# Kernel tuning notes

Hardware: AMD Instinct MI355X
Metric: run time of the kernel (lower is better)

The kernel has to match this reference:

```python
import jax, jax.numpy as jnp
import numpy as np
from jax import lax

B, L, H, I, Z = 1024, 128, 256, 32, 128  # batch, max_length, hidden, input_size, latent


def setup_inputs() -> dict:
    key = jax.random.key(0)
    ks = jax.random.split(key, 32)
    p = lambda k, shape: (jax.random.normal(k, shape, dtype=jnp.float32) * 0.05)
    d = {
        "x": jax.random.normal(ks[0], (B, Z), dtype=jnp.float32),
        "W1": p(ks[1], (512, Z)), "b1": p(ks[2], (512,)),
        "W2": p(ks[3], (512, 512)), "b2": p(ks[4], (512,)),
        "W3": p(ks[5], (512, 512)), "b3": p(ks[6], (512,)),
        # predict_h / predict_c / predict_x_0 heads
        "Wh1": p(ks[7], (512, 512)), "bh1": p(ks[8], (512,)),
        "Wh2": p(ks[9], (H, 512)), "bh2": p(ks[10], (H,)),
        "Wc1": p(ks[11], (512, 512)), "bc1": p(ks[12], (512,)),
        "Wc2": p(ks[13], (H, 512)), "bc2": p(ks[14], (H,)),
        "Wx1": p(ks[15], (512, 512)), "bx1": p(ks[16], (512,)),
        "Wx2": p(ks[17], (H, 512)), "bx2": p(ks[18], (H,)),
        # decode LSTM (input H -> hidden H), PyTorch gate order i,f,g,o
        "rWih": p(ks[19], (4 * H, H)), "rWhh": p(ks[20], (4 * H, H)),
        "rbih": p(ks[21], (4 * H,)), "rbhh": p(ks[22], (4 * H,)),
        # predictor LSTM (input H -> hidden I)
        "pWih": p(ks[23], (4 * I, H)), "pWhh": p(ks[24], (4 * I, I)),
        "pbih": p(ks[25], (4 * I,)), "pbhh": p(ks[26], (4 * I,)),
    }
    return d


def _leaky(v):
    return jnp.where(v >= 0, v, 0.2 * v)


def _lstm_cell(xt, h, c, Wih, Whh, b):
    gates = xt @ Wih.T + h @ Whh.T + b  # [B, 4G]
    i, f, g, o = jnp.split(gates, 4, axis=-1)
    c_new = jax.nn.sigmoid(f) * c + jax.nn.sigmoid(i) * jnp.tanh(g)
    h_new = jax.nn.sigmoid(o) * jnp.tanh(c_new)
    return h_new, c_new


def _forward(x, W1, b1, W2, b2, W3, b3, Wh1, bh1, Wh2, bh2, Wc1, bc1, Wc2, bc2,
             Wx1, bx1, Wx2, bx2, rWih, rWhh, rbih, rbhh, pWih, pWhh, pbih, pbhh):
    t = _leaky(x @ W1.T + b1)
    t = _leaky(t @ W2.T + b2)
    t = _leaky(t @ W3.T + b3)
    h = _leaky(t @ Wh1.T + bh1) @ Wh2.T + bh2   # [B, H]
    c = _leaky(t @ Wc1.T + bc1) @ Wc2.T + bc2   # [B, H]
    x0 = _leaky(t @ Wx1.T + bx1) @ Wx2.T + bx2  # [B, H]

    rb = rbih + rbhh
    # The torch loop re-feeds the growing sequence through the LSTM from the
    # same initial (h, c) each step; deterministically this equals a single
    # O(L) self-feeding scan: token_{i} = h-output of step i, fed at step i+1.
    def dec_step(carry, _):
        tok, hh, cc = carry
        h2, c2 = _lstm_cell(tok, hh, cc, rWih, rWhh, rb)
        return (h2, h2, c2), h2

    _, outs = lax.scan(dec_step, (x0, h, c), None, length=L)  # [L, B, H]

    pb = pbih + pbhh
    def pred_step(carry, xt):
        hh, cc = carry
        hh, cc = _lstm_cell(xt, hh, cc, pWih, pWhh, pb)
        return (hh, cc), hh

    h0 = jnp.zeros((B, I), dtype=x.dtype)
    _, pouts = lax.scan(pred_step, (h0, h0), outs)  # [L, B, I]
    y = jnp.transpose(pouts, (1, 0, 2))  # [B, L, I]

    layer_type = jax.nn.softmax(y[..., : I - 1], axis=-1)
    features = jax.nn.sigmoid(y[..., I - 1:])
    return jnp.concatenate([layer_type, features], axis=-1)


def reference(x, W1, b1, W2, b2, W3, b3, Wh1, bh1, Wh2, bh2, Wc1, bc1, Wc2, bc2,
              Wx1, bx1, Wx2, bx2, rWih, rWhh, rbih, rbhh, pWih, pWhh, pbih, pbhh):
    return _forward(x, W1, b1, W2, b2, W3, b3, Wh1, bh1, Wh2, bh2, Wc1, bc1, Wc2, bc2,
                    Wx1, bx1, Wx2, bx2, rWih, rWhh, rbih, rbhh, pWih, pWhh, pbih, pbhh)
```

## Files before the change

kernel.cpp:

```cpp
#include <hip/hip_runtime.h>
#include <hip/hip_fp8.h>

typedef unsigned short u16;
typedef unsigned char u8;
typedef __attribute__((ext_vector_type(8))) __bf16 bfrag;
typedef long long f8frag;
typedef __attribute__((ext_vector_type(4))) float f32x4;

static __device__ __forceinline__ f32x4 MFMA(bfrag a, bfrag b, f32x4 c) {
  return __builtin_amdgcn_mfma_f32_16x16x32_bf16(a, b, c, 0, 0, 0);
}
static __device__ __forceinline__ f32x4 MFMA8(f8frag a, f8frag b, f32x4 c) {
  return __builtin_amdgcn_mfma_f32_16x16x32_fp8_fp8(a, b, c, 0, 0, 0);
}

static __device__ __forceinline__ u16 f2b(float f) {
  union { float f; unsigned u; } v; v.f = f;
  unsigned r = (v.u + 0x7fffu + ((v.u >> 16) & 1u)) >> 16;
  return (u16)r;
}
static __device__ __forceinline__ u8 f2e4m3(float f) {
  return (u8)(__builtin_amdgcn_cvt_pk_fp8_f32(f, f, 0, false) & 0xff);
}
static __device__ __forceinline__ unsigned pk4_e4m3(float a, float b, float c, float d) {
  int p = __builtin_amdgcn_cvt_pk_fp8_f32(a, b, 0, false);
  p = __builtin_amdgcn_cvt_pk_fp8_f32(c, d, p, true);
  return (unsigned)p;
}
static __device__ __forceinline__ float rcp(float x) { return __builtin_amdgcn_rcpf(x); }
static __device__ __forceinline__ float ssig(float x) {
  float E = __expf(x);
  return E * rcp(1.f + E);
}
static __device__ __forceinline__ float2 lstm2(float gi, float gf, float gg,
                                               float go, float c) {
  float Ei = __expf(gi), Ef = __expf(gf), Eg = __expf(2.f * gg), Eo = __expf(go);
  float P = 1.f + Ef, Q = 1.f + Ei, R = 1.f + Eg;
  float QR = Q * R;
  float num = c * Ef * QR + Ei * P * (Eg - 1.f);
  float cn = num * rcp(P * QR);
  float Ec = __expf(2.f * cn);
  float hn = Eo * (Ec - 1.f) * rcp((1.f + Eo) * (Ec + 1.f));
  return make_float2(hn, cn);
}

#define LDS_BARRIER() asm volatile("s_waitcnt lgkmcnt(0)\ns_barrier" ::: "memory")
#define PIN_A8(A) asm volatile("" : "+a"(A[0]), "+a"(A[1]), "+a"(A[2]), "+a"(A[3]), \
                                    "+a"(A[4]), "+a"(A[5]), "+a"(A[6]), "+a"(A[7]))
#define PIN_V8(A) asm volatile("" : "+v"(A[0]), "+v"(A[1]), "+v"(A[2]), "+v"(A[3]), \
                                    "+v"(A[4]), "+v"(A[5]), "+v"(A[6]), "+v"(A[7]))

struct PrepArgs {
  const float *x, *W1, *W2, *W3, *Wh1, *Wc1, *Wx1, *Wh2, *Wc2, *Wx2;
  const float *rWih, *rWhh, *rbih, *rbhh, *pWih, *pWhh, *pbih, *pbhh;
  u16 *Xbf, *W1b, *W2b, *W3b, *Wh1b, *Wc1b, *Wx1b, *Wh2b, *Wc2b, *Wx2b;
  u16 *WcatR;
  u8 *WsS, *pWsS, *pWhhS;
  float *rbR, *pbR;
};

static __device__ __forceinline__ void emit_stream(u16* dst, const float* src,
                                                   int i, int K, int ktbits) {
  int j = i & 7, lane = (i >> 3) & 63;
  int kt = (i >> 9) & ((1 << ktbits) - 1);
  int nt = (i >> (9 + ktbits)) & 3;
  int ct = i >> (11 + ktbits);
  int srow = ct * 64 + nt * 16 + (lane & 15);
  int scol = kt * 32 + ((lane >> 4) & 3) * 8 + j;
  dst[i] = f2b(src[srow * K + scol]);
}

__global__ __launch_bounds__(256) void prep(PrepArgs p) {
  const int tid0 = blockIdx.x * 256 + threadIdx.x;
  const int stride = gridDim.x * 256;
  switch (blockIdx.y) {
    case 0: for (int i = tid0; i < 131072; i += stride) p.Xbf[i] = f2b(p.x[i]); break;
    case 1: for (int i = tid0; i < 65536;  i += stride) emit_stream(p.W1b, p.W1, i, 128, 2); break;
    case 2: for (int i = tid0; i < 262144; i += stride) emit_stream(p.W2b, p.W2, i, 512, 4); break;
    case 3: for (int i = tid0; i < 262144; i += stride) emit_stream(p.W3b, p.W3, i, 512, 4); break;
    case 4: for (int i = tid0; i < 262144; i += stride) emit_stream(p.Wh1b, p.Wh1, i, 512, 4); break;
    case 5: for (int i = tid0; i < 262144; i += stride) emit_stream(p.Wc1b, p.Wc1, i, 512, 4); break;
    case 6: for (int i = tid0; i < 262144; i += stride) emit_stream(p.Wx1b, p.Wx1, i, 512, 4); break;
    case 7: for (int i = tid0; i < 131072; i += stride) emit_stream(p.Wh2b, p.Wh2, i, 512, 4); break;
    case 8: for (int i = tid0; i < 131072; i += stride) emit_stream(p.Wc2b, p.Wc2, i, 512, 4); break;
    case 9: for (int i = tid0; i < 131072; i += stride) emit_stream(p.Wx2b, p.Wx2, i, 512, 4); break;
    case 10:
      for (int i = tid0; i < 524288; i += stride) {
        int j = i & 7, lane = (i >> 3) & 63, kt = (i >> 9) & 15;
        int gate = (i >> 13) & 3, w16 = i >> 15;
        int srow = gate * 256 + w16 * 16 + (lane & 15);
        int k = kt * 32 + ((lane >> 4) & 3) * 8 + j;
        float v = (k < 256) ? p.rWih[srow * 256 + k] : p.rWhh[srow * 256 + (k - 256)];
        p.WcatR[i] = f2b(v);
      }
      break;
    case 11:
      for (int i = tid0; i < 1024; i += stride) {
        int srow = (((i >> 4) & 3) << 8) + ((i >> 6) << 4) + (i & 15);
        p.rbR[i] = p.rbih[srow] + p.rbhh[srow];
      }
      break;
    case 12:
      for (int i = tid0; i < 32768; i += stride) {
        int j = i & 7, lane = (i >> 3) & 63, kt = (i >> 9) & 7, w = i >> 12;
        int n = w * 16 + (lane & 15);
        int srow = ((n & 3) << 5) + (n >> 2);
        int k = kt * 32 + ((lane >> 4) & 3) * 8 + j;
        p.pWsS[i] = f2e4m3(p.pWih[srow * 256 + k]);
      }
      break;
    case 13:
      for (int i = tid0; i < 4096; i += stride) {
        int j = i & 7, lane = (i >> 3) & 63, w = i >> 9;
        int n = w * 16 + (lane & 15);
        int srow = ((n & 3) << 5) + (n >> 2);
        int k = ((lane >> 4) & 3) * 8 + j;
        p.pWhhS[i] = f2e4m3(p.pWhh[srow * 32 + k]);
      }
      break;
    case 14:
      for (int i = tid0; i < 128; i += stride) {
        int srow = ((i & 3) << 5) + (i >> 2);
        p.pbR[i] = p.pbih[srow] + p.pbhh[srow];
      }
      break;
    case 15:
      for (int i = tid0; i < 262144; i += stride) {
        int j = i & 7, lane = (i >> 3) & 63, kt = (i >> 9) & 7;
        int gate = (i >> 12) & 3, g16 = i >> 14;
        int srow = gate * 256 + g16 * 16 + (lane & 15);
        int k = kt * 32 + ((lane >> 4) & 3) * 8 + j;
        p.WsS[i] = f2e4m3(p.rWih[srow * 256 + k] + p.rWhh[srow * 256 + k]);
      }
      break;
  }
}

__global__ __launch_bounds__(256) void gemm_act(
    const u16* __restrict__ X, const u16* __restrict__ W,
    const float* __restrict__ bias,
    u16* __restrict__ Yb, float* __restrict__ Yf,
    int K, int ldo, int coloff, int leaky) {
  const int rt = blockIdx.x, ct = blockIdx.y;
  const int lane = threadIdx.x & 63, wave = threadIdx.x >> 6;
  const int m15 = lane & 15, q = lane >> 4, kq = q * 8;
  const int KT = K >> 5;
  const int row = rt * 64 + wave * 16 + m15;
  f32x4 acc[4] = {};
  const u16* xp = X + (size_t)row * K + kq;
  const u16* wst = W + lane * 8;
  for (int kt = 0; kt < KT; kt++) {
    bfrag a = *(const bfrag*)(xp + kt * 32);
#pragma unroll
    for (int nt = 0; nt < 4; nt++) {
      const u16* wp = wst + (size_t)((ct * 4 + nt) * KT + kt) * 512;
      acc[nt] = MFMA(a, *(const bfrag*)wp, acc[nt]);
    }
  }
#pragma unroll
  for (int nt = 0; nt < 4; nt++) {
    int col = ct * 64 + nt * 16 + m15;
    float bv = bias[col];
#pragma unroll
    for (int r = 0; r < 4; r++) {
      int orow = rt * 64 + wave * 16 + q * 4 + r;
      float v = acc[nt][r] + bv;
      if (leaky) v = v >= 0.f ? v : 0.2f * v;
      if (Yb) Yb[(size_t)orow * ldo + coloff + col] = f2b(v);
      else    Yf[(size_t)orow * ldo + coloff + col] = v;
    }
  }
}

struct G3 {
  const u16 *X, *W;
  const float* bias;
  u16* Yb;
  float* Yf;
  int K, ldo, coloff, leaky;
};
__global__ __launch_bounds__(256) void gemm_act3(G3 ga, G3 gb, G3 gc) {
  G3 g = (blockIdx.z == 0) ? ga : (blockIdx.z == 1) ? gb : gc;
  const int rt = blockIdx.x, ct = blockIdx.y;
  const int lane = threadIdx.x & 63, wave = threadIdx.x >> 6;
  const int m15 = lane & 15, q = lane >> 4, kq = q * 8;
  const int KT = g.K >> 5;
  const int row = rt * 64 + wave * 16 + m15;
  f32x4 acc[4] = {};
  const u16* xp = g.X + (size_t)row * g.K + kq;
  const u16* wst = g.W + lane * 8;
  for (int kt = 0; kt < KT; kt++) {
    bfrag a = *(const bfrag*)(xp + kt * 32);
#pragma unroll
    for (int nt = 0; nt < 4; nt++) {
      const u16* wp = wst + (size_t)((ct * 4 + nt) * KT + kt) * 512;
      acc[nt] = MFMA(a, *(const bfrag*)wp, acc[nt]);
    }
  }
#pragma unroll
  for (int nt = 0; nt < 4; nt++) {
    int col = ct * 64 + nt * 16 + m15;
    float bv = g.bias[col];
#pragma unroll
    for (int r = 0; r < 4; r++) {
      int orow = rt * 64 + wave * 16 + q * 4 + r;
      float v = acc[nt][r] + bv;
      if (g.leaky) v = v >= 0.f ? v : 0.2f * v;
      if (g.Yb) g.Yb[(size_t)orow * g.ldo + g.coloff + col] = f2b(v);
      else      g.Yf[(size_t)orow * g.ldo + g.coloff + col] = v;
    }
  }
}

__global__ __attribute__((amdgpu_flat_work_group_size(1024, 1024), amdgpu_waves_per_eu(4, 4)))
void decode_h(
    const u8* __restrict__ WsS,
    const u16* __restrict__ WcatR,
    const float* __restrict__ rb,
    const float* __restrict__ CB,
    const u16* __restrict__ X0H,
    u8* __restrict__ hG) {
  __shared__ __align__(16) u8 hbufS[2][4096];
  __shared__ __align__(16) u8 WoL[16][4096];
  const int tid = threadIdx.x;
  const int w = tid >> 6, lane = tid & 63;
  const int m15 = lane & 15, q = lane >> 4;
  const int b = blockIdx.x;
  const int rowg = b * 16;

  {
    int4* dst = (int4*)WoL;
    for (int i = tid; i < 4096; i += 1024) {
      int wv = i >> 8, rest = i & 255;
      dst[i] = ((const int4*)(WsS + wv * 16384 + 12288))[rest];
    }
  }
  const float* rbp = rb + w * 64 + q * 4;
  f32x4 rbv0 = *(const f32x4*)(rbp +  0);
  f32x4 rbv1 = *(const f32x4*)(rbp + 16);
  f32x4 rbv2 = *(const f32x4*)(rbp + 32);
  f32x4 rbv3 = *(const f32x4*)(rbp + 48);
  asm volatile("" : "+v"(rbv0), "+v"(rbv1), "+v"(rbv2), "+v"(rbv3));
  f32x4 cst = *(const f32x4*)(CB + (size_t)(rowg + m15) * 256 + w * 16 + q * 4);
  const int wroff = (w >> 1) * 512 + ((w & 1) * 2 + (q >> 1)) * 128 + m15 * 8 + (q & 1) * 4;
  u8* hGs = hG + (size_t)b * 524288 + wroff;

  {
    f32x4 ai = rbv0, af_ = rbv1, ag = rbv2, ao = rbv3;
    const u16* xrow = X0H + (size_t)(rowg + m15) * 512 + q * 8;
    const u16* wcw = WcatR + (size_t)w * 32768 + lane * 8;
#pragma unroll
    for (int kt = 0; kt < 16; kt++) {
      bfrag a = *(const bfrag*)(xrow + kt * 32);
      ai  = MFMA(*(const bfrag*)(wcw + kt * 512), a, ai);
      af_ = MFMA(*(const bfrag*)(wcw + 8192 + kt * 512), a, af_);
      ag  = MFMA(*(const bfrag*)(wcw + 16384 + kt * 512), a, ag);
      ao  = MFMA(*(const bfrag*)(wcw + 24576 + kt * 512), a, ao);
    }
    float hn[4];
#pragma unroll
    for (int r = 0; r < 4; r++) {
      float2 hc2 = lstm2(ai[r], af_[r], ag[r], ao[r], cst[r]);
      hn[r] = hc2.x;
      cst[r] = hc2.y;
    }
    unsigned hv = pk4_e4m3(hn[0], hn[1], hn[2], hn[3]);
    *(unsigned*)(&hbufS[0][wroff]) = hv;
    *(unsigned*)hGs = hv;
  }
  const u8* wsb = WsS + (size_t)w * 16384 + lane * 8;
  f8frag Wv0[8], Wv1[8], Wv2[8];
#pragma unroll
  for (int kt = 0; kt < 8; kt++) {
    Wv0[kt] = *(const f8frag*)(wsb + kt * 512);
    Wv1[kt] = *(const f8frag*)(wsb + 4096 + kt * 512);
    Wv2[kt] = *(const f8frag*)(wsb + 8192 + kt * 512);
  }
  PIN_A8(Wv0); PIN_A8(Wv1); PIN_A8(Wv2);
  const u8* woW = &WoL[w][lane * 8];
  __syncthreads();

  for (int s = 1; s < 128; s++) {
    PIN_A8(Wv0); PIN_A8(Wv1); PIN_A8(Wv2);
    asm volatile("" : "+v"(rbv0), "+v"(rbv1), "+v"(rbv2), "+v"(rbv3));
    const u8* h8 = &hbufS[(s - 1) & 1][lane * 8];
    f32x4 ai = rbv0, af_ = rbv1, ag = rbv2, ao = rbv3;
#pragma unroll
    for (int kt = 0; kt < 8; kt++) {
      f8frag a8 = *(const f8frag*)(h8 + kt * 512);
      f8frag wo = *(const f8frag*)(woW + kt * 512);
      ai  = MFMA8(Wv0[kt], a8, ai);
      af_ = MFMA8(Wv1[kt], a8, af_);
      ag  = MFMA8(Wv2[kt], a8, ag);
      ao  = MFMA8(wo, a8, ao);
    }
    float hn[4];
#pragma unroll
    for (int r = 0; r < 4; r++) {
      float2 hc2 = lstm2(ai[r], af_[r], ag[r], ao[r], cst[r]);
      hn[r] = hc2.x;
      cst[r] = hc2.y;
    }
    unsigned hv = pk4_e4m3(hn[0], hn[1], hn[2], hn[3]);
    *(unsigned*)(&hbufS[s & 1][wroff]) = hv;
    *(unsigned*)(hGs + (size_t)s * 4096) = hv;
    LDS_BARRIER();
  }
}

__global__ __launch_bounds__(512, 2) void pred_y(
    const u8* __restrict__ hG,
    const u8* __restrict__ pWsS,
    const u8* __restrict__ pWhhS,
    const float* __restrict__ pb,
    float* __restrict__ out) {
  __shared__ __align__(16) u8 stageL[16384];
  __shared__ __align__(16) u8 hp8[2][16][40];
  __shared__ float ysC[4][16][36];
  const int tid = threadIdx.x;
  const int w = tid >> 6, lane = tid & 63;
  const int m15 = lane & 15, q = lane >> 4;
  const int b = blockIdx.x, rowg = b * 16;
  for (int i = tid; i < 2 * 16 * 40; i += 512) (&hp8[0][0][0])[i] = 0;
  const u8* pwsb = pWsS + (size_t)w * 4096 + lane * 8;
  f8frag pbv[8];
#pragma unroll
  for (int kt = 0; kt < 8; kt++) pbv[kt] = *(const f8frag*)(pwsb + kt * 512);
  f8frag phw = *(const f8frag*)(pWhhS + (size_t)w * 512 + lane * 8);
  PIN_V8(pbv);
  asm volatile("" : "+v"(phw));
  const f32x4 pbias = *(const f32x4*)(pb + w * 16 + q * 4);
  float cp = 0.f;
  const int4* hGb = (const int4*)(hG + (size_t)b * 524288);
  const int t_si = (tid >> 3) >> 4, t_r = (tid >> 3) & 15, sub = tid & 7;
  __syncthreads();

  for (int cs = 0; cs < 32; cs++) {
    {
      int4* sdst = (int4*)stageL;
      sdst[tid] = hGb[cs * 1024 + tid];
      sdst[tid + 512] = hGb[cs * 1024 + tid + 512];
    }
    __syncthreads();
#pragma unroll
    for (int si = 0; si < 4; si++) {
      const int s = cs * 4 + si;
      const u8* xr8 = &stageL[si * 4096 + lane * 8];
      f32x4 pacc = pbias;
#pragma unroll
      for (int kt = 0; kt < 8; kt++) {
        f8frag pav = *(const f8frag*)(xr8 + kt * 512);
        pacc = MFMA8(pbv[kt], pav, pacc);
      }
      f8frag pah = *(const f8frag*)(&hp8[s & 1][m15][q * 8]);
      pacc = MFMA8(phw, pah, pacc);
      float2 hc2 = lstm2(pacc[0], pacc[1], pacc[2], pacc[3], cp);
      cp = hc2.y;
      hp8[(s + 1) & 1][m15][w * 4 + q] = f2e4m3(hc2.x);
      ysC[si][m15][w * 4 + q] = hc2.x;
      LDS_BARRIER();
    }
    {
      f32x4 yv = *(const f32x4*)&ysC[t_si][t_r][sub * 4];
      float v3 = (sub == 7) ? -1e30f : yv[3];
      float m = fmaxf(fmaxf(yv[0], yv[1]), fmaxf(yv[2], v3));
#pragma unroll
      for (int off = 4; off; off >>= 1) m = fmaxf(m, __shfl_xor(m, off, 8));
      float e0 = __expf(yv[0] - m), e1 = __expf(yv[1] - m), e2 = __expf(yv[2] - m);
      float e3 = (sub == 7) ? 0.f : __expf(yv[3] - m);
      float tot = e0 + e1 + e2 + e3;
#pragma unroll
      for (int off = 4; off; off >>= 1) tot += __shfl_xor(tot, off, 8);
      float inv = rcp(tot);
      f32x4 o;
      o[0] = e0 * inv; o[1] = e1 * inv; o[2] = e2 * inv;
      o[3] = (sub == 7) ? ssig(yv[3]) : e3 * inv;
      *(f32x4*)(out + (size_t)(rowg + t_r) * 4096 + (cs * 4 + t_si) * 32 + sub * 4) = o;
    }
    LDS_BARRIER();
  }
}

extern "C" void kernel_launch(void* const* d_in, const int* in_sizes, int n_in,
                              void* d_out, int out_size, void* d_ws, size_t ws_size,
                              hipStream_t stream) {
  (void)in_sizes; (void)n_in; (void)out_size; (void)ws_size;
  const float* x    = (const float*)d_in[0];
  const float* W1   = (const float*)d_in[1];
  const float* b1   = (const float*)d_in[2];
  const float* W2   = (const float*)d_in[3];
  const float* b2   = (const float*)d_in[4];
  const float* W3   = (const float*)d_in[5];
  const float* b3   = (const float*)d_in[6];
  const float* Wh1  = (const float*)d_in[7];
  const float* bh1  = (const float*)d_in[8];
  const float* Wh2  = (const float*)d_in[9];
  const float* bh2  = (const float*)d_in[10];
  const float* Wc1  = (const float*)d_in[11];
  const float* bc1  = (const float*)d_in[12];
  const float* Wc2  = (const float*)d_in[13];
  const float* bc2  = (const float*)d_in[14];
  const float* Wx1  = (const float*)d_in[15];
  const float* bx1  = (const float*)d_in[16];
  const float* Wx2  = (const float*)d_in[17];
  const float* bx2  = (const float*)d_in[18];
  const float* rWih = (const float*)d_in[19];
  const float* rWhh = (const float*)d_in[20];
  const float* rbih = (const float*)d_in[21];
  const float* rbhh = (const float*)d_in[22];
  const float* pWih = (const float*)d_in[23];
  const float* pWhh = (const float*)d_in[24];
  const float* pbih = (const float*)d_in[25];
  const float* pbhh = (const float*)d_in[26];

  char* w = (char*)d_ws;
  auto alloc = [&](size_t bytes) -> char* {
    char* p = w;
    w += (bytes + 255) & ~(size_t)255;
    return p;
  };
  u16* Xbf  = (u16*)alloc(1024 * 128 * 2);
  u16* T1   = (u16*)alloc(1024 * 512 * 2);
  u16* T2   = (u16*)alloc(1024 * 512 * 2);
  u16* T3   = (u16*)alloc(1024 * 512 * 2);
  u16* TH   = (u16*)alloc(1024 * 512 * 2);
  u16* TC   = (u16*)alloc(1024 * 512 * 2);
  u16* TX   = (u16*)alloc(1024 * 512 * 2);
  u16* X0H  = (u16*)alloc(1024 * 512 * 2);
  float* CB = (float*)alloc(1024 * 256 * 4);
  u16* W1b  = (u16*)alloc(512 * 128 * 2);
  u16* W2b  = (u16*)alloc(512 * 512 * 2);
  u16* W3b  = (u16*)alloc(512 * 512 * 2);
  u16* Wh1b = (u16*)alloc(512 * 512 * 2);
  u16* Wc1b = (u16*)alloc(512 * 512 * 2);
  u16* Wx1b = (u16*)alloc(512 * 512 * 2);
  u16* Wh2b = (u16*)alloc(256 * 512 * 2);
  u16* Wc2b = (u16*)alloc(256 * 512 * 2);
  u16* Wx2b = (u16*)alloc(256 * 512 * 2);
  u16* WcatR= (u16*)alloc(1024 * 512 * 2);
  u8*  WsS  = (u8*)alloc(262144);
  u8*  pWsS = (u8*)alloc(32768);
  u8*  pWhhS= (u8*)alloc(4096);
  float* rbR = (float*)alloc(1024 * 4);
  float* pbR = (float*)alloc(128 * 4);
  u8*  hG   = (u8*)alloc((size_t)64 * 128 * 4096);

  PrepArgs pa;
  pa.x = x; pa.W1 = W1; pa.W2 = W2; pa.W3 = W3; pa.Wh1 = Wh1; pa.Wc1 = Wc1; pa.Wx1 = Wx1;
  pa.Wh2 = Wh2; pa.Wc2 = Wc2; pa.Wx2 = Wx2;
  pa.rWih = rWih; pa.rWhh = rWhh; pa.rbih = rbih; pa.rbhh = rbhh;
  pa.pWih = pWih; pa.pWhh = pWhh; pa.pbih = pbih; pa.pbhh = pbhh;
  pa.Xbf = Xbf; pa.W1b = W1b; pa.W2b = W2b; pa.W3b = W3b; pa.Wh1b = Wh1b;
  pa.Wc1b = Wc1b; pa.Wx1b = Wx1b; pa.Wh2b = Wh2b; pa.Wc2b = Wc2b; pa.Wx2b = Wx2b;
  pa.WcatR = WcatR;
  pa.WsS = WsS; pa.pWsS = pWsS; pa.pWhhS = pWhhS;
  pa.rbR = rbR; pa.pbR = pbR;
  prep<<<dim3(32, 16), 256, 0, stream>>>(pa);

  gemm_act<<<dim3(16, 8), 256, 0, stream>>>(Xbf, W1b, b1, T1, nullptr, 128, 512, 0, 1);
  gemm_act<<<dim3(16, 8), 256, 0, stream>>>(T1, W2b, b2, T2, nullptr, 512, 512, 0, 1);
  gemm_act<<<dim3(16, 8), 256, 0, stream>>>(T2, W3b, b3, T3, nullptr, 512, 512, 0, 1);
  G3 h1a = {T3, Wh1b, bh1, TH, nullptr, 512, 512, 0, 1};
  G3 h1b = {T3, Wc1b, bc1, TC, nullptr, 512, 512, 0, 1};
  G3 h1c = {T3, Wx1b, bx1, TX, nullptr, 512, 512, 0, 1};
  gemm_act3<<<dim3(16, 8, 3), 256, 0, stream>>>(h1a, h1b, h1c);
  G3 h2a = {TH, Wh2b, bh2, X0H, nullptr, 512, 512, 256, 0};
  G3 h2b = {TC, Wc2b, bc2, nullptr, CB, 512, 256, 0, 0};
  G3 h2c = {TX, Wx2b, bx2, X0H, nullptr, 512, 512, 0, 0};
  gemm_act3<<<dim3(16, 4, 3), 256, 0, stream>>>(h2a, h2b, h2c);

  decode_h<<<64, 1024, 0, stream>>>(WsS, WcatR, rbR, CB, X0H, hG);
  pred_y<<<64, 512, 0, stream>>>(hG, pWsS, pWhhS, pbR, (float*)d_out);
}
```

Before: 487.3 us.

## Fuse MLP trunk and heads into decode kernel using swizzled LDS activations

Removes the five separate GEMM launches and instead computes the whole MLP trunk plus the h/c/x0 heads inside the decode_h kernel. Each block handles its 16 rows, and intermediate activations ping-pong through XOR-swizzled shared-memory buffers instead of global memory. The initial c state stays in registers, and the x0/h concatenation is written straight to LDS. This saves launch overhead and global round trips. In exchange, only 64 blocks do all the MLP work, so every block re-reads all the MLP weights from global or cache.

```diff
diff --git a/kernel.cpp b/kernel.cpp
--- a/kernel.cpp
+++ b/kernel.cpp
@@ -6,6 +6,7 @@
 typedef __attribute__((ext_vector_type(8))) __bf16 bfrag;
 typedef long long f8frag;
 typedef __attribute__((ext_vector_type(4))) float f32x4;
+typedef __attribute__((ext_vector_type(4))) unsigned short u16x4;
 
 static __device__ __forceinline__ f32x4 MFMA(bfrag a, bfrag b, f32x4 c) {
   return __builtin_amdgcn_mfma_f32_16x16x32_bf16(a, b, c, 0, 0, 0);
@@ -49,6 +50,10 @@
                                     "+a"(A[4]), "+a"(A[5]), "+a"(A[6]), "+a"(A[7]))
 #define PIN_V8(A) asm volatile("" : "+v"(A[0]), "+v"(A[1]), "+v"(A[2]), "+v"(A[3]), \
                                     "+v"(A[4]), "+v"(A[5]), "+v"(A[6]), "+v"(A[7]))
+
+static __device__ __forceinline__ int sw(int r, int byteoff) {
+  return r * 1024 + (byteoff ^ ((r & 7) << 4));
+}
 
 struct PrepArgs {
   const float *x, *W1, *W2, *W3, *Wh1, *Wc1, *Wx1, *Wh2, *Wc2, *Wx2;
@@ -136,92 +141,64 @@
   }
 }
 
-__global__ __launch_bounds__(256) void gemm_act(
-    const u16* __restrict__ X, const u16* __restrict__ W,
+template<int NT, int KT, bool AG, bool OL>
+static __device__ __forceinline__ void mlayer(
+    const u16* __restrict__ Ag,
+    const u8* __restrict__ Al,
+    u8* __restrict__ Ol,
+    int cobyte,
+    f32x4* accOut,
+    const u16* __restrict__ Wst,
     const float* __restrict__ bias,
-    u16* __restrict__ Yb, float* __restrict__ Yf,
-    int K, int ldo, int coloff, int leaky) {
-  const int rt = blockIdx.x, ct = blockIdx.y;
-  const int lane = threadIdx.x & 63, wave = threadIdx.x >> 6;
-  const int m15 = lane & 15, q = lane >> 4, kq = q * 8;
-  const int KT = K >> 5;
-  const int row = rt * 64 + wave * 16 + m15;
-  f32x4 acc[4] = {};
-  const u16* xp = X + (size_t)row * K + kq;
-  const u16* wst = W + lane * 8;
+    int w, int m15, int q, int leaky) {
+  f32x4 acc[NT];
+#pragma unroll
+  for (int nt = 0; nt < NT; nt++)
+    acc[nt] = *(const f32x4*)(bias + (w * NT + nt) * 16 + q * 4);
+#pragma unroll
   for (int kt = 0; kt < KT; kt++) {
-    bfrag a = *(const bfrag*)(xp + kt * 32);
-#pragma unroll
-    for (int nt = 0; nt < 4; nt++) {
-      const u16* wp = wst + (size_t)((ct * 4 + nt) * KT + kt) * 512;
-      acc[nt] = MFMA(a, *(const bfrag*)wp, acc[nt]);
-    }
-  }
-#pragma unroll
-  for (int nt = 0; nt < 4; nt++) {
-    int col = ct * 64 + nt * 16 + m15;
-    float bv = bias[col];
-#pragma unroll
-    for (int r = 0; r < 4; r++) {
-      int orow = rt * 64 + wave * 16 + q * 4 + r;
-      float v = acc[nt][r] + bv;
-      if (leaky) v = v >= 0.f ? v : 0.2f * v;
-      if (Yb) Yb[(size_t)orow * ldo + coloff + col] = f2b(v);
-      else    Yf[(size_t)orow * ldo + coloff + col] = v;
-    }
-  }
-}
-
-struct G3 {
-  const u16 *X, *W;
-  const float* bias;
-  u16* Yb;
-  float* Yf;
-  int K, ldo, coloff, leaky;
+    bfrag a;
+    if (AG) a = *(const bfrag*)(Ag + kt * 32);
+    else    a = *(const bfrag*)(Al + sw(m15, kt * 64 + q * 16));
+#pragma unroll
+    for (int nt = 0; nt < NT; nt++) {
+      bfrag wv = *(const bfrag*)(Wst + (size_t)(((w * NT + nt) * KT + kt) << 9));
+      acc[nt] = MFMA(wv, a, acc[nt]);
+    }
+  }
+#pragma unroll
+  for (int nt = 0; nt < NT; nt++) {
+    if (leaky) {
+#pragma unroll
+      for (int r = 0; r < 4; r++)
+        acc[nt][r] = acc[nt][r] >= 0.f ? acc[nt][r] : 0.2f * acc[nt][r];
+    }
+    if (OL) {
+      u16x4 pk;
+#pragma unroll
+      for (int r = 0; r < 4; r++) pk[r] = f2b(acc[nt][r]);
+      *(u16x4*)(Ol + sw(m15, cobyte + ((w * NT + nt) * 16 + q * 4) * 2)) = pk;
+    } else {
+      accOut[nt] = acc[nt];
+    }
+  }
+}
+
+struct MegaArgs {
+  const u8* WsS; const u16* WcatR; const float* rb;
+  const u16* Xbf;
+  const u16 *W1b, *W2b, *W3b, *Wh1b, *Wh2b, *Wc1b, *Wc2b, *Wx1b, *Wx2b;
+  const float *b1, *b2, *b3, *bh1, *bh2, *bc1, *bc2, *bx1, *bx2;
+  u8* hG;
 };
-__global__ __launch_bounds__(256) void gemm_act3(G3 ga, G3 gb, G3 gc) {
-  G3 g = (blockIdx.z == 0) ? ga : (blockIdx.z == 1) ? gb : gc;
-  const int rt = blockIdx.x, ct = blockIdx.y;
-  const int lane = threadIdx.x & 63, wave = threadIdx.x >> 6;
-  const int m15 = lane & 15, q = lane >> 4, kq = q * 8;
-  const int KT = g.K >> 5;
-  const int row = rt * 64 + wave * 16 + m15;
-  f32x4 acc[4] = {};
-  const u16* xp = g.X + (size_t)row * g.K + kq;
-  const u16* wst = g.W + lane * 8;
-  for (int kt = 0; kt < KT; kt++) {
-    bfrag a = *(const bfrag*)(xp + kt * 32);
-#pragma unroll
-    for (int nt = 0; nt < 4; nt++) {
-      const u16* wp = wst + (size_t)((ct * 4 + nt) * KT + kt) * 512;
-      acc[nt] = MFMA(a, *(const bfrag*)wp, acc[nt]);
-    }
-  }
-#pragma unroll
-  for (int nt = 0; nt < 4; nt++) {
-    int col = ct * 64 + nt * 16 + m15;
-    float bv = g.bias[col];
-#pragma unroll
-    for (int r = 0; r < 4; r++) {
-      int orow = rt * 64 + wave * 16 + q * 4 + r;
-      float v = acc[nt][r] + bv;
-      if (g.leaky) v = v >= 0.f ? v : 0.2f * v;
-      if (g.Yb) g.Yb[(size_t)orow * g.ldo + g.coloff + col] = f2b(v);
-      else      g.Yf[(size_t)orow * g.ldo + g.coloff + col] = v;
-    }
-  }
-}
 
 __global__ __attribute__((amdgpu_flat_work_group_size(1024, 1024), amdgpu_waves_per_eu(4, 4)))
-void decode_h(
-    const u8* __restrict__ WsS,
-    const u16* __restrict__ WcatR,
-    const float* __restrict__ rb,
-    const float* __restrict__ CB,
-    const u16* __restrict__ X0H,
-    u8* __restrict__ hG) {
+void decode_h(MegaArgs p) {
   __shared__ __align__(16) u8 hbufS[2][4096];
   __shared__ __align__(16) u8 WoL[16][4096];
+  __shared__ __align__(16) u8 bufA[16384];
+  __shared__ __align__(16) u8 bufB[16384];
+  __shared__ __align__(16) u8 xh[16384];
   const int tid = threadIdx.x;
   const int w = tid >> 6, lane = tid & 63;
   const int m15 = lane & 15, q = lane >> 4;
@@ -232,26 +209,61 @@
     int4* dst = (int4*)WoL;
     for (int i = tid; i < 4096; i += 1024) {
       int wv = i >> 8, rest = i & 255;
-      dst[i] = ((const int4*)(WsS + wv * 16384 + 12288))[rest];
-    }
-  }
-  const float* rbp = rb + w * 64 + q * 4;
+      dst[i] = ((const int4*)(p.WsS + wv * 16384 + 12288))[rest];
+    }
+  }
+
+  const u16* wl8 = (const u16*)nullptr;
+  f32x4 cst;
+  {
+    const u16* Ag1 = p.Xbf + (size_t)(rowg + m15) * 128 + q * 8;
+    mlayer<2, 4, true, true>(Ag1, nullptr, bufA, 0, nullptr,
+                             p.W1b + lane * 8, p.b1, w, m15, q, 1);
+    LDS_BARRIER();
+    mlayer<2, 16, false, true>(nullptr, bufA, bufB, 0, nullptr,
+                               p.W2b + lane * 8, p.b2, w, m15, q, 1);
+    LDS_BARRIER();
+    mlayer<2, 16, false, true>(nullptr, bufB, bufA, 0, nullptr,
+                               p.W3b + lane * 8, p.b3, w, m15, q, 1);
+    LDS_BARRIER();
+    mlayer<2, 16, false, true>(nullptr, bufA, bufB, 0, nullptr,
+                               p.Wh1b + lane * 8, p.bh1, w, m15, q, 1);
+    LDS_BARRIER();
+    mlayer<1, 16, false, true>(nullptr, bufB, xh, 512, nullptr,
+                               p.Wh2b + lane * 8, p.bh2, w, m15, q, 0);
+    LDS_BARRIER();
+    mlayer<2, 16, false, true>(nullptr, bufA, bufB, 0, nullptr,
+                               p.Wc1b + lane * 8, p.bc1, w, m15, q, 1);
+    LDS_BARRIER();
+    f32x4 cacc[1];
+    mlayer<1, 16, false, false>(nullptr, bufB, nullptr, 0, cacc,
+                                p.Wc2b + lane * 8, p.bc2, w, m15, q, 0);
+    cst = cacc[0];
+    LDS_BARRIER();
+    mlayer<2, 16, false, true>(nullptr, bufA, bufB, 0, nullptr,
+                               p.Wx1b + lane * 8, p.bx1, w, m15, q, 1);
+    LDS_BARRIER();
+    mlayer<1, 16, false, true>(nullptr, bufB, xh, 0, nullptr,
+                               p.Wx2b + lane * 8, p.bx2, w, m15, q, 0);
+    LDS_BARRIER();
+  }
+  (void)wl8;
+
+  const float* rbp = p.rb + w * 64 + q * 4;
   f32x4 rbv0 = *(const f32x4*)(rbp +  0);
   f32x4 rbv1 = *(const f32x4*)(rbp + 16);
   f32x4 rbv2 = *(const f32x4*)(rbp + 32);
   f32x4 rbv3 = *(const f32x4*)(rbp + 48);
   asm volatile("" : "+v"(rbv0), "+v"(rbv1), "+v"(rbv2), "+v"(rbv3));
-  f32x4 cst = *(const f32x4*)(CB + (size_t)(rowg + m15) * 256 + w * 16 + q * 4);
   const int wroff = (w >> 1) * 512 + ((w & 1) * 2 + (q >> 1)) * 128 + m15 * 8 + (q & 1) * 4;
-  u8* hGs = hG + (size_t)b * 524288 + wroff;
+  u8* hGs = p.hG + (size_t)b * 524288 + wroff;
 
   {
     f32x4 ai = rbv0, af_ = rbv1, ag = rbv2, ao = rbv3;
-    const u16* xrow = X0H + (size_t)(rowg + m15) * 512 + q * 8;
-    const u16* wcw = WcatR + (size_t)w * 32768 + lane * 8;
+    const u16* wcw = p.WcatR + (size_t)w * 32768 + lane * 8;
 #pragma unroll
     for (int kt = 0; kt < 16; kt++) {
-      bfrag a = *(const bfrag*)(xrow + kt * 32);
+      bfrag a = *(const bfrag*)(xh + sw(m15, kt * 64 + q * 16));
       ai  = MFMA(*(const bfrag*)(wcw + kt * 512), a, ai);
       af_ = MFMA(*(const bfrag*)(wcw + 8192 + kt * 512), a, af_);
       ag  = MFMA(*(const bfrag*)(wcw + 16384 + kt * 512), a, ag);
@@ -268,7 +280,7 @@
     *(unsigned*)(&hbufS[0][wroff]) = hv;
     *(unsigned*)hGs = hv;
   }
-  const u8* wsb = WsS + (size_t)w * 16384 + lane * 8;
+  const u8* wsb = p.WsS + (size_t)w * 16384 + lane * 8;
   f8frag Wv0[8], Wv1[8], Wv2[8];
 #pragma unroll
   for (int kt = 0; kt < 8; kt++) {
@@ -420,14 +432,6 @@
     return p;
   };
   u16* Xbf  = (u16*)alloc(1024 * 128 * 2);
-  u16* T1   = (u16*)alloc(1024 * 512 * 2);
-  u16* T2   = (u16*)alloc(1024 * 512 * 2);
-  u16* T3   = (u16*)alloc(1024 * 512 * 2);
-  u16* TH   = (u16*)alloc(1024 * 512 * 2);
-  u16* TC   = (u16*)alloc(1024 * 512 * 2);
-  u16* TX   = (u16*)alloc(1024 * 512 * 2);
-  u16* X0H  = (u16*)alloc(1024 * 512 * 2);
-  float* CB = (float*)alloc(1024 * 256 * 4);
   u16* W1b  = (u16*)alloc(512 * 128 * 2);
   u16* W2b  = (u16*)alloc(512 * 512 * 2);
   u16* W3b  = (u16*)alloc(512 * 512 * 2);
@@ -457,18 +461,16 @@
   pa.rbR = rbR; pa.pbR = pbR;
   prep<<<dim3(32, 16), 256, 0, stream>>>(pa);
 
-  gemm_act<<<dim3(16, 8), 256, 0, stream>>>(Xbf, W1b, b1, T1, nullptr, 128, 512, 0, 1);
-  gemm_act<<<dim3(16, 8), 256, 0, stream>>>(T1, W2b, b2, T2, nullptr, 512, 512, 0, 1);
-  gemm_act<<<dim3(16, 8), 256, 0, stream>>>(T2, W3b, b3, T3, nullptr, 512, 512, 0, 1);
-  G3 h1a = {T3, Wh1b, bh1, TH, nullptr, 512, 512, 0, 1};
-  G3 h1b = {T3, Wc1b, bc1, TC, nullptr, 512, 512, 0, 1};
-  G3 h1c = {T3, Wx1b, bx1, TX, nullptr, 512, 512, 0, 1};
-  gemm_act3<<<dim3(16, 8, 3), 256, 0, stream>>>(h1a, h1b, h1c);
-  G3 h2a = {TH, Wh2b, bh2, X0H, nullptr, 512, 512, 256, 0};
-  G3 h2b = {TC, Wc2b, bc2, nullptr, CB, 512, 256, 0, 0};
-  G3 h2c = {TX, Wx2b, bx2, X0H, nullptr, 512, 512, 0, 0};
-  gemm_act3<<<dim3(16, 4, 3), 256, 0, stream>>>(h2a, h2b, h2c);
-
-  decode_h<<<64, 1024, 0, stream>>>(WsS, WcatR, rbR, CB, X0H, hG);
+  MegaArgs ma;
+  ma.WsS = WsS; ma.WcatR = WcatR; ma.rb = rbR;
+  ma.Xbf = Xbf;
+  ma.W1b = W1b; ma.W2b = W2b; ma.W3b = W3b;
+  ma.Wh1b = Wh1b; ma.Wh2b = Wh2b; ma.Wc1b = Wc1b; ma.Wc2b = Wc2b;
+  ma.Wx1b = Wx1b; ma.Wx2b = Wx2b;
+  ma.b1 = b1; ma.b2 = b2; ma.b3 = b3; ma.bh1 = bh1; ma.bh2 = bh2;
+  ma.bc1 = bc1; ma.bc2 = bc2; ma.bx1 = bx1; ma.bx2 = bx2;
+  ma.hG = hG;
+
+  decode_h<<<64, 1024, 0, stream>>>(ma);
   pred_y<<<64, 512, 0, stream>>>(hG, pWsS, pWhhS, pbR, (float*)d_out);
 }
```

Measured after the change: 532.3 us. 9.2% more time.

## Fuse decode and predictor LSTMs into one kernel with flag-based producer/consumer overlap

Applied to the files above, without the earlier changes.

Merges the decode LSTM and predictor LSTM kernels into a single 128-block launch. Blocks 0-63 run the decode recurrence and publish a per-block progress flag every four steps. Blocks 64-127 spin on that flag and consume the hidden states while decoding is still running, so the two sequential recurrences overlap instead of running back to back. This depends on all 128 blocks being co-resident, or the spin-waits deadlock. It also adds atomic loads and stores, and the predictor blocks now run at 1024 threads with half the waves idle.

```diff
diff --git a/kernel.cpp b/kernel.cpp
--- a/kernel.cpp
+++ b/kernel.cpp
@@ -57,6 +57,7 @@
   u16 *WcatR;
   u8 *WsS, *pWsS, *pWhhS;
   float *rbR, *pbR;
+  unsigned *flags;
 };
 
 static __device__ __forceinline__ void emit_stream(u16* dst, const float* src,
@@ -123,6 +124,8 @@
         int srow = ((i & 3) << 5) + (i >> 2);
         p.pbR[i] = p.pbih[srow] + p.pbhh[srow];
       }
+      for (int i = tid0; i < 64; i += stride)
+        __hip_atomic_store(p.flags + i, 0u, __ATOMIC_RELAXED, __HIP_MEMORY_SCOPE_AGENT);
       break;
     case 15:
       for (int i = tid0; i < 262144; i += stride) {
@@ -213,171 +216,188 @@
 }
 
 __global__ __attribute__((amdgpu_flat_work_group_size(1024, 1024), amdgpu_waves_per_eu(4, 4)))
-void decode_h(
+void decode_pred(
     const u8* __restrict__ WsS,
     const u16* __restrict__ WcatR,
     const float* __restrict__ rb,
     const float* __restrict__ CB,
     const u16* __restrict__ X0H,
-    u8* __restrict__ hG) {
-  __shared__ __align__(16) u8 hbufS[2][4096];
-  __shared__ __align__(16) u8 WoL[16][4096];
-  const int tid = threadIdx.x;
-  const int w = tid >> 6, lane = tid & 63;
-  const int m15 = lane & 15, q = lane >> 4;
-  const int b = blockIdx.x;
-  const int rowg = b * 16;
-
-  {
-    int4* dst = (int4*)WoL;
-    for (int i = tid; i < 4096; i += 1024) {
-      int wv = i >> 8, rest = i & 255;
-      dst[i] = ((const int4*)(WsS + wv * 16384 + 12288))[rest];
-    }
-  }
-  const float* rbp = rb + w * 64 + q * 4;
-  f32x4 rbv0 = *(const f32x4*)(rbp +  0);
-  f32x4 rbv1 = *(const f32x4*)(rbp + 16);
-  f32x4 rbv2 = *(const f32x4*)(rbp + 32);
-  f32x4 rbv3 = *(const f32x4*)(rbp + 48);
-  asm volatile("" : "+v"(rbv0), "+v"(rbv1), "+v"(rbv2), "+v"(rbv3));
-  f32x4 cst = *(const f32x4*)(CB + (size_t)(rowg + m15) * 256 + w * 16 + q * 4);
-  const int wroff = (w >> 1) * 512 + ((w & 1) * 2 + (q >> 1)) * 128 + m15 * 8 + (q & 1) * 4;
-  u8* hGs = hG + (size_t)b * 524288 + wroff;
-
-  {
-    f32x4 ai = rbv0, af_ = rbv1, ag = rbv2, ao = rbv3;
-    const u16* xrow = X0H + (size_t)(rowg + m15) * 512 + q * 8;
-    const u16* wcw = WcatR + (size_t)w * 32768 + lane * 8;
-#pragma unroll
-    for (int kt = 0; kt < 16; kt++) {
-      bfrag a = *(const bfrag*)(xrow + kt * 32);
-      ai  = MFMA(*(const bfrag*)(wcw + kt * 512), a, ai);
-      af_ = MFMA(*(const bfrag*)(wcw + 8192 + kt * 512), a, af_);
-      ag  = MFMA(*(const bfrag*)(wcw + 16384 + kt * 512), a, ag);
-      ao  = MFMA(*(const bfrag*)(wcw + 24576 + kt * 512), a, ao);
-    }
-    float hn[4];
-#pragma unroll
-    for (int r = 0; r < 4; r++) {
-      float2 hc2 = lstm2(ai[r], af_[r], ag[r], ao[r], cst[r]);
-      hn[r] = hc2.x;
-      cst[r] = hc2.y;
-    }
-    unsigned hv = pk4_e4m3(hn[0], hn[1], hn[2], hn[3]);
-    *(unsigned*)(&hbufS[0][wroff]) = hv;
-    *(unsigned*)hGs = hv;
-  }
-  const u8* wsb = WsS + (size_t)w * 16384 + lane * 8;
-  f8frag Wv0[8], Wv1[8], Wv2[8];
-#pragma unroll
-  for (int kt = 0; kt < 8; kt++) {
-    Wv0[kt] = *(const f8frag*)(wsb + kt * 512);
-    Wv1[kt] = *(const f8frag*)(wsb + 4096 + kt * 512);
-    Wv2[kt] = *(const f8frag*)(wsb + 8192 + kt * 512);
-  }
-  PIN_A8(Wv0); PIN_A8(Wv1); PIN_A8(Wv2);
-  const u8* woW = &WoL[w][lane * 8];
-  __syncthreads();
-
-  for (int s = 1; s < 128; s++) {
-    PIN_A8(Wv0); PIN_A8(Wv1); PIN_A8(Wv2);
-    asm volatile("" : "+v"(rbv0), "+v"(rbv1), "+v"(rbv2), "+v"(rbv3));
-    const u8* h8 = &hbufS[(s - 1) & 1][lane * 8];
-    f32x4 ai = rbv0, af_ = rbv1, ag = rbv2, ao = rbv3;
-#pragma unroll
-    for (int kt = 0; kt < 8; kt++) {
-      f8frag a8 = *(const f8frag*)(h8 + kt * 512);
-      f8frag wo = *(const f8frag*)(woW + kt * 512);
-      ai  = MFMA8(Wv0[kt], a8, ai);
-      af_ = MFMA8(Wv1[kt], a8, af_);
-      ag  = MFMA8(Wv2[kt], a8, ag);
-      ao  = MFMA8(wo, a8, ao);
-    }
-    float hn[4];
-#pragma unroll
-    for (int r = 0; r < 4; r++) {
-      float2 hc2 = lstm2(ai[r], af_[r], ag[r], ao[r], cst[r]);
-      hn[r] = hc2.x;
-      cst[r] = hc2.y;
-    }
-    unsigned hv = pk4_e4m3(hn[0], hn[1], hn[2], hn[3]);
-    *(unsigned*)(&hbufS[s & 1][wroff]) = hv;
-    *(unsigned*)(hGs + (size_t)s * 4096) = hv;
-    LDS_BARRIER();
-  }
-}
-
-__global__ __launch_bounds__(512, 2) void pred_y(
-    const u8* __restrict__ hG,
     const u8* __restrict__ pWsS,
     const u8* __restrict__ pWhhS,
     const float* __restrict__ pb,
-    float* __restrict__ out) {
+    float* __restrict__ out,
+    u8* __restrict__ hG,
+    unsigned* __restrict__ flags) {
+  __shared__ __align__(16) u8 hbufS[2][4096];
+  __shared__ __align__(16) u8 WoL[16][4096];
   __shared__ __align__(16) u8 stageL[16384];
   __shared__ __align__(16) u8 hp8[2][16][40];
   __shared__ float ysC[4][16][36];
   const int tid = threadIdx.x;
   const int w = tid >> 6, lane = tid & 63;
   const int m15 = lane & 15, q = lane >> 4;
-  const int b = blockIdx.x, rowg = b * 16;
-  for (int i = tid; i < 2 * 16 * 40; i += 512) (&hp8[0][0][0])[i] = 0;
-  const u8* pwsb = pWsS + (size_t)w * 4096 + lane * 8;
-  f8frag pbv[8];
-#pragma unroll
-  for (int kt = 0; kt < 8; kt++) pbv[kt] = *(const f8frag*)(pwsb + kt * 512);
-  f8frag phw = *(const f8frag*)(pWhhS + (size_t)w * 512 + lane * 8);
-  PIN_V8(pbv);
-  asm volatile("" : "+v"(phw));
-  const f32x4 pbias = *(const f32x4*)(pb + w * 16 + q * 4);
-  float cp = 0.f;
-  const int4* hGb = (const int4*)(hG + (size_t)b * 524288);
-  const int t_si = (tid >> 3) >> 4, t_r = (tid >> 3) & 15, sub = tid & 7;
-  __syncthreads();
-
-  for (int cs = 0; cs < 32; cs++) {
+
+  if (blockIdx.x < 64) {
+    const int b = blockIdx.x;
+    const int rowg = b * 16;
     {
-      int4* sdst = (int4*)stageL;
-      sdst[tid] = hGb[cs * 1024 + tid];
-      sdst[tid + 512] = hGb[cs * 1024 + tid + 512];
-    }
+      int4* dst = (int4*)WoL;
+      for (int i = tid; i < 4096; i += 1024) {
+        int wv = i >> 8, rest = i & 255;
+        dst[i] = ((const int4*)(WsS + wv * 16384 + 12288))[rest];
+      }
+    }
+    const float* rbp = rb + w * 64 + q * 4;
+    f32x4 rbv0 = *(const f32x4*)(rbp +  0);
+    f32x4 rbv1 = *(const f32x4*)(rbp + 16);
+    f32x4 rbv2 = *(const f32x4*)(rbp + 32);
+    f32x4 rbv3 = *(const f32x4*)(rbp + 48);
+    asm volatile("" : "+v"(rbv0), "+v"(rbv1), "+v"(rbv2), "+v"(rbv3));
+    f32x4 cst = *(const f32x4*)(CB + (size_t)(rowg + m15) * 256 + w * 16 + q * 4);
+    const int wroff = (w >> 1) * 512 + ((w & 1) * 2 + (q >> 1)) * 128 + m15 * 8 + (q & 1) * 4;
+    u8* hGs = hG + (size_t)b * 524288 + wroff;
+
+    {
+      f32x4 ai = rbv0, af_ = rbv1, ag = rbv2, ao = rbv3;
+      const u16* xrow = X0H + (size_t)(rowg + m15) * 512 + q * 8;
+      const u16* wcw = WcatR + (size_t)w * 32768 + lane * 8;
+#pragma unroll
+      for (int kt = 0; kt < 16; kt++) {
+        bfrag a = *(const bfrag*)(xrow + kt * 32);
+        ai  = MFMA(*(const bfrag*)(wcw + kt * 512), a, ai);
+        af_ = MFMA(*(const bfrag*)(wcw + 8192 + kt * 512), a, af_);
+        ag  = MFMA(*(const bfrag*)(wcw + 16384 + kt * 512), a, ag);
+        ao  = MFMA(*(const bfrag*)(wcw + 24576 + kt * 512), a, ao);
+      }
+      float hn[4];
+#pragma unroll
+      for (int r = 0; r < 4; r++) {
+        float2 hc2 = lstm2(ai[r], af_[r], ag[r], ao[r], cst[r]);
+        hn[r] = hc2.x;
+        cst[r] = hc2.y;
+      }
+      unsigned hv = pk4_e4m3(hn[0], hn[1], hn[2], hn[3]);
+      *(unsigned*)(&hbufS[0][wroff]) = hv;
+      __hip_atomic_store((unsigned*)hGs, hv, __ATOMIC_RELAXED, __HIP_MEMORY_SCOPE_AGENT);
+    }
+    const u8* wsb = WsS + (size_t)w * 16384 + lane * 8;
+    f8frag Wv0[8], Wv1[8], Wv2[8];
+#pragma unroll
+    for (int kt = 0; kt < 8; kt++) {
+      Wv0[kt] = *(const f8frag*)(wsb + kt * 512);
+      Wv1[kt] = *(const f8frag*)(wsb + 4096 + kt * 512);
+      Wv2[kt] = *(const f8frag*)(wsb + 8192 + kt * 512);
+    }
+    PIN_A8(Wv0); PIN_A8(Wv1); PIN_A8(Wv2);
+    const u8* woW = &WoL[w][lane * 8];
     __syncthreads();
-#pragma unroll
-    for (int si = 0; si < 4; si++) {
-      const int s = cs * 4 + si;
-      const u8* xr8 = &stageL[si * 4096 + lane * 8];
-      f32x4 pacc = pbias;
+
+    for (int s = 1; s < 128; s++) {
+      PIN_A8(Wv0); PIN_A8(Wv1); PIN_A8(Wv2);
+      asm volatile("" : "+v"(rbv0), "+v"(rbv1), "+v"(rbv2), "+v"(rbv3));
+      const u8* h8 = &hbufS[(s - 1) & 1][lane * 8];
+      f32x4 ai = rbv0, af_ = rbv1, ag = rbv2, ao = rbv3;
 #pragma unroll
       for (int kt = 0; kt < 8; kt++) {
-        f8frag pav = *(const f8frag*)(xr8 + kt * 512);
-        pacc = MFMA8(pbv[kt], pav, pacc);
-      }
-      f8frag pah = *(const f8frag*)(&hp8[s & 1][m15][q * 8]);
-      pacc = MFMA8(phw, pah, pacc);
-      float2 hc2 = lstm2(pacc[0], pacc[1], pacc[2], pacc[3], cp);
-      cp = hc2.y;
-      hp8[(s + 1) & 1][m15][w * 4 + q] = f2e4m3(hc2.x);
-      ysC[si][m15][w * 4 + q] = hc2.x;
+        f8frag a8 = *(const f8frag*)(h8 + kt * 512);
+        f8frag wo = *(const f8frag*)(woW + kt * 512);
+        ai  = MFMA8(Wv0[kt], a8, ai);
+        af_ = MFMA8(Wv1[kt], a8, af_);
+        ag  = MFMA8(Wv2[kt], a8, ag);
+        ao  = MFMA8(wo, a8, ao);
+      }
+      float hn[4];
+#pragma unroll
+      for (int r = 0; r < 4; r++) {
+        float2 hc2 = lstm2(ai[r], af_[r], ag[r], ao[r], cst[r]);
+        hn[r] = hc2.x;
+        cst[r] = hc2.y;
+      }
+      unsigned hv = pk4_e4m3(hn[0], hn[1], hn[2], hn[3]);
+      *(unsigned*)(&hbufS[s & 1][wroff]) = hv;
+      __hip_atomic_store((unsigned*)(hGs + (size_t)s * 4096), hv,
+                         __ATOMIC_RELAXED, __HIP_MEMORY_SCOPE_AGENT);
+      if ((s & 3) == 3) {
+        __syncthreads();
+        if (tid == 0)
+          __hip_atomic_store(flags + b, (unsigned)((s >> 2) + 1),
+                             __ATOMIC_RELEASE, __HIP_MEMORY_SCOPE_AGENT);
+      } else {
+        LDS_BARRIER();
+      }
+    }
+  } else {
+    const int b = blockIdx.x - 64;
+    const int rowg = b * 16;
+    for (int i = tid; i < 2 * 16 * 40; i += 1024) (&hp8[0][0][0])[i] = 0;
+    const u8* pwsb = pWsS + (size_t)(w & 7) * 4096 + lane * 8;
+    f8frag pbv[8];
+#pragma unroll
+    for (int kt = 0; kt < 8; kt++) pbv[kt] = *(const f8frag*)(pwsb + kt * 512);
+    f8frag phw = *(const f8frag*)(pWhhS + (size_t)(w & 7) * 512 + lane * 8);
+    PIN_V8(pbv);
+    asm volatile("" : "+v"(phw));
+    const f32x4 pbias = *(const f32x4*)(pb + (w & 7) * 16 + q * 4);
+    float cp = 0.f;
+    const u8* hGc = hG + (size_t)b * 524288;
+    const int t_si = (tid >> 3) >> 4, t_r = (tid >> 3) & 15, sub = tid & 7;
+
+    for (int cs = 0; cs < 32; cs++) {
+      if (tid == 0) {
+        while (__hip_atomic_load(flags + b, __ATOMIC_ACQUIRE,
+                                 __HIP_MEMORY_SCOPE_AGENT) < (unsigned)(cs + 1))
+          __builtin_amdgcn_s_sleep(2);
+      }
+      __syncthreads();
+      {
+        const unsigned* src = (const unsigned*)(hGc + (size_t)cs * 16384) + tid * 4;
+        unsigned d0 = __hip_atomic_load(src + 0, __ATOMIC_RELAXED, __HIP_MEMORY_SCOPE_AGENT);
+        unsigned d1 = __hip_atomic_load(src + 1, __ATOMIC_RELAXED, __HIP_MEMORY_SCOPE_AGENT);
+        unsigned d2 = __hip_atomic_load(src + 2, __ATOMIC_RELAXED, __HIP_MEMORY_SCOPE_AGENT);
+        unsigned d3 = __hip_atomic_load(src + 3, __ATOMIC_RELAXED, __HIP_MEMORY_SCOPE_AGENT);
+        int4 vv; vv.x = d0; vv.y = d1; vv.z = d2; vv.w = d3;
+        *(int4*)&stageL[tid * 16] = vv;
+      }
+      __syncthreads();
+#pragma unroll
+      for (int si = 0; si < 4; si++) {
+        const int s = cs * 4 + si;
+        if (w < 8) {
+          const u8* xr8 = &stageL[si * 4096 + lane * 8];
+          f32x4 pacc = pbias;
+#pragma unroll
+          for (int kt = 0; kt < 8; kt++) {
+            f8frag pav = *(const f8frag*)(xr8 + kt * 512);
+            pacc = MFMA8(pbv[kt], pav, pacc);
+          }
+          f8frag pah = *(const f8frag*)(&hp8[s & 1][m15][q * 8]);
+          pacc = MFMA8(phw, pah, pacc);
+          float2 hc2 = lstm2(pacc[0], pacc[1], pacc[2], pacc[3], cp);
+          cp = hc2.y;
+          hp8[(s + 1) & 1][m15][w * 4 + q] = f2e4m3(hc2.x);
+          ysC[si][m15][w * 4 + q] = hc2.x;
+        }
+        LDS_BARRIER();
+      }
+      if (tid < 512) {
+        f32x4 yv = *(const f32x4*)&ysC[t_si][t_r][sub * 4];
+        float v3 = (sub == 7) ? -1e30f : yv[3];
+        float m = fmaxf(fmaxf(yv[0], yv[1]), fmaxf(yv[2], v3));
+#pragma unroll
+        for (int off = 4; off; off >>= 1) m = fmaxf(m, __shfl_xor(m, off, 8));
+        float e0 = __expf(yv[0] - m), e1 = __expf(yv[1] - m), e2 = __expf(yv[2] - m);
+        float e3 = (sub == 7) ? 0.f : __expf(yv[3] - m);
+        float tot = e0 + e1 + e2 + e3;
+#pragma unroll
+        for (int off = 4; off; off >>= 1) tot += __shfl_xor(tot, off, 8);
+        float inv = rcp(tot);
+        f32x4 o;
+        o[0] = e0 * inv; o[1] = e1 * inv; o[2] = e2 * inv;
+        o[3] = (sub == 7) ? ssig(yv[3]) : e3 * inv;
+        *(f32x4*)(out + (size_t)(rowg + t_r) * 4096 + (cs * 4 + t_si) * 32 + sub * 4) = o;
+      }
       LDS_BARRIER();
     }
-    {
-      f32x4 yv = *(const f32x4*)&ysC[t_si][t_r][sub * 4];
-      float v3 = (sub == 7) ? -1e30f : yv[3];
-      float m = fmaxf(fmaxf(yv[0], yv[1]), fmaxf(yv[2], v3));
-#pragma unroll
-      for (int off = 4; off; off >>= 1) m = fmaxf(m, __shfl_xor(m, off, 8));
-      float e0 = __expf(yv[0] - m), e1 = __expf(yv[1] - m), e2 = __expf(yv[2] - m);
-      float e3 = (sub == 7) ? 0.f : __expf(yv[3] - m);
-      float tot = e0 + e1 + e2 + e3;
-#pragma unroll
-      for (int off = 4; off; off >>= 1) tot += __shfl_xor(tot, off, 8);
-      float inv = rcp(tot);
-      f32x4 o;
-      o[0] = e0 * inv; o[1] = e1 * inv; o[2] = e2 * inv;
-      o[3] = (sub == 7) ? ssig(yv[3]) : e3 * inv;
-      *(f32x4*)(out + (size_t)(rowg + t_r) * 4096 + (cs * 4 + t_si) * 32 + sub * 4) = o;
-    }
-    LDS_BARRIER();
   }
 }
 
@@ -443,6 +463,7 @@
   u8*  pWhhS= (u8*)alloc(4096);
   float* rbR = (float*)alloc(1024 * 4);
   float* pbR = (float*)alloc(128 * 4);
+  unsigned* flags = (unsigned*)alloc(64 * 4);
   u8*  hG   = (u8*)alloc((size_t)64 * 128 * 4096);
 
   PrepArgs pa;
@@ -455,6 +476,7 @@
   pa.WcatR = WcatR;
   pa.WsS = WsS; pa.pWsS = pWsS; pa.pWhhS = pWhhS;
   pa.rbR = rbR; pa.pbR = pbR;
+  pa.flags = flags;
   prep<<<dim3(32, 16), 256, 0, stream>>>(pa);
 
   gemm_act<<<dim3(16, 8), 256, 0, stream>>>(Xbf, W1b, b1, T1, nullptr, 128, 512, 0, 1);
@@ -469,6 +491,7 @@
   G3 h2c = {TX, Wx2b, bx2, X0H, nullptr, 512, 512, 0, 0};
   gemm_act3<<<dim3(16, 4, 3), 256, 0, stream>>>(h2a, h2b, h2c);
 
-  decode_h<<<64, 1024, 0, stream>>>(WsS, WcatR, rbR, CB, X0H, hG);
-  pred_y<<<64, 512, 0, stream>>>(hG, pWsS, pWhhS, pbR, (float*)d_out);
-}
+  decode_pred<<<128, 1024, 0, stream>>>(WsS, WcatR, rbR, CB, X0H,
+                                        pWsS, pWhhS, pbR,
+                                        (float*)d_out, hG, flags);
+}
```

New measurement: 459.0 us (median of 2 runs). 5.8% less time.
